# Kernel tuning notes

Measured on AMD Instinct MI355X. Metric: run time of the kernel, lower is better.

Reference implementation:

```python
import jax, jax.numpy as jnp
import numpy as np

B, H, W, C = 16, 32, 32, 256
N = H * W


def setup_inputs() -> dict:
    key = jax.random.key(0)
    ks = jax.random.split(key, 8)
    x = jax.random.normal(ks[0], (B, H, W, C), dtype=jnp.float32)
    # nn.LazyLinear(C): weight (C, C), bias (C,)
    scale = 1.0 / np.sqrt(C)
    Wq = jax.random.uniform(ks[1], (C, C), jnp.float32, -scale, scale)
    bq = jax.random.uniform(ks[2], (C,), jnp.float32, -scale, scale)
    Wk = jax.random.uniform(ks[3], (C, C), jnp.float32, -scale, scale)
    bk = jax.random.uniform(ks[4], (C,), jnp.float32, -scale, scale)
    Wv = jax.random.uniform(ks[5], (C, C), jnp.float32, -scale, scale)
    bv = jax.random.uniform(ks[6], (C,), jnp.float32, -scale, scale)
    # torch.randn(H, H*W, W)
    Wp = jax.random.normal(ks[7], (H, N, W), dtype=jnp.float32)
    return {"x": x, "Wq": Wq, "bq": bq, "Wk": Wk, "bk": bk,
            "Wv": Wv, "bv": bv, "Wp": Wp}


def reference(x, Wq, bq, Wk, bk, Wv, bv, Wp):
    b, h, w, c = x.shape
    n = h * w
    # Linear projections (torch Linear: x @ W^T + b), flatten spatial dims to N tokens
    q = (jnp.einsum('bhwc,dc->bhwd', x, Wq) + bq).reshape(b, n, c)
    k = (jnp.einsum('bhwc,dc->bhwd', x, Wk) + bk).reshape(b, n, c)
    v = (jnp.einsum('bhwc,dc->bhwd', x, Wv) + bv).reshape(b, n, c)
    # Unscaled attention over the N spatial tokens (no 1/sqrt(C) in the original)
    scores = jnp.einsum('bnc,bmc->bnm', q, k)          # (B, N, N)
    attn = jax.nn.softmax(scores, axis=-1)
    qkv = jnp.einsum('bnm,bmc->bnc', attn, v)           # (B, N, C)
    # z = (qkv^T [B,1,C,N] @ Wp [H,N,W]).transpose(-2,-1) -> (B, H, W, C)
    z = jnp.einsum('bnc,hnw->bhwc', qkv, Wp)
    return z
```

## Files before the change

### kernel.cpp

```cpp
#include <hip/hip_runtime.h>
#include <hip/hip_bf16.h>

#define BB 16
#define NN 1024
#define CC 256

typedef __attribute__((ext_vector_type(8))) short bf16x8;
typedef __attribute__((ext_vector_type(4))) float f32x4;

#define GPTR(p) ((const __attribute__((address_space(1))) void*)(p))
#define LPTR(p) ((__attribute__((address_space(3))) void*)(p))

__device__ __forceinline__ unsigned short f2bf(float f) {
  union { float f; unsigned u; } v; v.f = f;
  unsigned r = v.u + 0x7FFFu + ((v.u >> 16) & 1u);
  return (unsigned short)(r >> 16);
}

#define NCAST 17155
__global__ __launch_bounds__(256) void preprocess(
    const float* __restrict__ x,
    const float* __restrict__ Wq, const float* __restrict__ Wk,
    const float* __restrict__ Wv,
    const float* __restrict__ bq, const float* __restrict__ bk,
    const float* __restrict__ bv,
    const float* __restrict__ Wp,
    unsigned short* __restrict__ xb,
    unsigned short* __restrict__ wqkvb,
    float* __restrict__ bqkv,
    unsigned short* __restrict__ Amat) {
  __shared__ float tile[32][33];
  int blk = blockIdx.x;
  if (blk < NCAST) {
    const int NX = BB * NN * CC;
    const int NW = CC * CC;
    int i = blk * 256 + threadIdx.x;
    if (i < NX) { xb[i] = f2bf(x[i]); return; }
    int j = i - NX;
    if (j < 3 * NW) {
      const float* w = (j < NW) ? Wq : (j < 2 * NW ? Wk : Wv);
      wqkvb[j] = f2bf(w[j % NW]);
      return;
    }
    int jj = j - 3 * NW;
    if (jj < 3 * CC) {
      const float* bb = (jj < CC) ? bq : (jj < 2 * CC ? bk : bv);
      bqkv[jj] = bb[jj % CC];
    }
    return;
  }
  int wb = blk - NCAST;
  int h = wb >> 5;
  int n0 = (wb & 31) * 32;
#pragma unroll
  for (int j = 0; j < 4; j++) {
    int idx = threadIdx.x + j * 256;
    int a = idx >> 5, wc = idx & 31;
    tile[a][wc] = Wp[(size_t)h * (NN * 32) + (size_t)(n0 + a) * 32 + wc];
  }
  __syncthreads();
#pragma unroll
  for (int j = 0; j < 4; j++) {
    int idx = threadIdx.x + j * 256;
    int wc = idx >> 5, a = idx & 31;
    Amat[(size_t)(h * 32 + wc) * NN + n0 + a] = f2bf(tile[a][wc]);
  }
}

template <int BIAS_MODE, int F32OUT>
__global__ __launch_bounds__(256) void gemm_tile(
    const unsigned short* __restrict__ A, int lda, long sA,
    const unsigned short* __restrict__ Bt, int ldb, long sB,
    const float* __restrict__ bias,
    void* __restrict__ Out, int ldo, long sO, int K) {
  __shared__ unsigned short As[2 * 128 * 32];
  __shared__ unsigned short Bs[2 * 64 * 32];
  int b = blockIdx.x;
  int m0 = blockIdx.y * 128;
  int n0 = blockIdx.z * 64;
  int t = threadIdx.x;
  int w = t >> 6, lane = t & 63;
  int wm = (w >> 1) * 64, wn = (w & 1) * 32;
  int r = lane & 15, g = lane >> 4;

  const unsigned short* Ab = A + (long)b * sA;
  const unsigned short* Bb = Bt + (long)b * sB;

  int srow = t >> 2;
  int scol = (t & 3) * 8;

  f32x4 acc[4][2];
#pragma unroll
  for (int i = 0; i < 4; i++)
#pragma unroll
    for (int j = 0; j < 2; j++) acc[i][j] = (f32x4){0.f, 0.f, 0.f, 0.f};

  for (int k0 = 0; k0 < K; k0 += 64) {
    __syncthreads();
#pragma unroll
    for (int kh = 0; kh < 2; kh++) {
#pragma unroll
      for (int jj = 0; jj < 2; jj++) {
        __builtin_amdgcn_global_load_lds(
            GPTR(Ab + (long)(m0 + srow + jj * 64) * lda + k0 + kh * 32 + scol),
            LPTR(&As[kh * 4096 + jj * 2048 + t * 8]), 16, 0, 0);
      }
      __builtin_amdgcn_global_load_lds(
          GPTR(Bb + (long)(n0 + srow) * ldb + k0 + kh * 32 + scol),
          LPTR(&Bs[kh * 2048 + t * 8]), 16, 0, 0);
    }
    __syncthreads();
#pragma unroll
    for (int kh = 0; kh < 2; kh++) {
      bf16x8 af[4], bfr[2];
#pragma unroll
      for (int ti = 0; ti < 4; ti++)
        af[ti] = *(const bf16x8*)&As[kh * 4096 + (wm + ti * 16 + r) * 32 + g * 8];
#pragma unroll
      for (int tj = 0; tj < 2; tj++)
        bfr[tj] = *(const bf16x8*)&Bs[kh * 2048 + (wn + tj * 16 + r) * 32 + g * 8];
#pragma unroll
      for (int ti = 0; ti < 4; ti++)
#pragma unroll
        for (int tj = 0; tj < 2; tj++)
          acc[ti][tj] = __builtin_amdgcn_mfma_f32_16x16x32_bf16(af[ti], bfr[tj], acc[ti][tj], 0, 0, 0);
    }
  }

#pragma unroll
  for (int ti = 0; ti < 4; ti++) {
#pragma unroll
    for (int tj = 0; tj < 2; tj++) {
      int col = n0 + wn + tj * 16 + r;
      float bc = (BIAS_MODE == 1) ? bias[col] : 0.0f;
#pragma unroll
      for (int rr = 0; rr < 4; rr++) {
        int row = m0 + wm + ti * 16 + g * 4 + rr;
        float val = acc[ti][tj][rr] + bc;
        long oidx = (long)b * sO + (long)row * ldo + col;
        if (F32OUT)
          ((float*)Out)[oidx] = val;
        else
          ((unsigned short*)Out)[oidx] = f2bf(val);
      }
    }
  }
}

__global__ __launch_bounds__(256) void gemm_qkv(
    const unsigned short* __restrict__ A,
    const unsigned short* __restrict__ Bt,
    const float* __restrict__ bias,
    unsigned short* __restrict__ Qb, unsigned short* __restrict__ Kb,
    unsigned short* __restrict__ Vtb) {
  __shared__ unsigned short As[2 * 128 * 32];
  __shared__ unsigned short Bs[2 * 128 * 32];
  int b = blockIdx.x;
  int m0 = blockIdx.y * 128;
  int n0 = blockIdx.z * 128;
  int t = threadIdx.x;
  int w = t >> 6, lane = t & 63;
  int wm = (w >> 1) * 64, wn = (w & 1) * 64;
  int r = lane & 15, g = lane >> 4;

  const unsigned short* Ab = A + (long)b * NN * CC;
  int srow = t >> 2;
  int scol = (t & 3) * 8;

  f32x4 acc[4][4];
#pragma unroll
  for (int i = 0; i < 4; i++)
#pragma unroll
    for (int j = 0; j < 4; j++) acc[i][j] = (f32x4){0.f, 0.f, 0.f, 0.f};

  for (int k0 = 0; k0 < CC; k0 += 64) {
    __syncthreads();
#pragma unroll
    for (int kh = 0; kh < 2; kh++) {
#pragma unroll
      for (int jj = 0; jj < 2; jj++) {
        __builtin_amdgcn_global_load_lds(
            GPTR(Ab + (long)(m0 + srow + jj * 64) * CC + k0 + kh * 32 + scol),
            LPTR(&As[kh * 4096 + jj * 2048 + t * 8]), 16, 0, 0);
        __builtin_amdgcn_global_load_lds(
            GPTR(Bt + (long)(n0 + srow + jj * 64) * CC + k0 + kh * 32 + scol),
            LPTR(&Bs[kh * 4096 + jj * 2048 + t * 8]), 16, 0, 0);
      }
    }
    __syncthreads();
#pragma unroll
    for (int kh = 0; kh < 2; kh++) {
      bf16x8 af[4], bfr[4];
#pragma unroll
      for (int ti = 0; ti < 4; ti++)
        af[ti] = *(const bf16x8*)&As[kh * 4096 + (wm + ti * 16 + r) * 32 + g * 8];
#pragma unroll
      for (int tj = 0; tj < 4; tj++)
        bfr[tj] = *(const bf16x8*)&Bs[kh * 4096 + (wn + tj * 16 + r) * 32 + g * 8];
#pragma unroll
      for (int ti = 0; ti < 4; ti++)
#pragma unroll
        for (int tj = 0; tj < 4; tj++)
          acc[ti][tj] = __builtin_amdgcn_mfma_f32_16x16x32_bf16(af[ti], bfr[tj], acc[ti][tj], 0, 0, 0);
    }
  }

  int seg = n0 >> 8;
#pragma unroll
  for (int ti = 0; ti < 4; ti++) {
#pragma unroll
    for (int tj = 0; tj < 4; tj++) {
      int col = n0 + wn + tj * 16 + r;
      int c = col & 255;
      float bc = bias[col];
#pragma unroll
      for (int rr = 0; rr < 4; rr++) {
        int row = m0 + wm + ti * 16 + g * 4 + rr;
        float val = acc[ti][tj][rr] + bc;
        long base = (long)b * NN * CC;
        if (seg == 0) {
          Qb[base + (long)row * CC + c] = f2bf(val);
        } else if (seg == 1) {
          Kb[base + ((long)(c >> 5) * NN + row) * 32 + (c & 31)] = f2bf(val);
        } else {
          Vtb[base + ((((long)(c >> 4) * 128 + (row >> 3)) * 16 + (c & 15)) * 8 + (row & 7))] = f2bf(val);
        }
      }
    }
  }
}

__global__ __launch_bounds__(512, 4) void attn_fused(
    const unsigned short* __restrict__ Q,
    const unsigned short* __restrict__ Kt,
    const unsigned short* __restrict__ Vt,
    unsigned short* __restrict__ QKVt) {
  __shared__ unsigned short ShBuf[32 * 1024];
  __shared__ float red[8][32];
  int b = blockIdx.x;
  int n0 = blockIdx.y * 32;
  int t = threadIdx.x;
  int w = t >> 6, lane = t & 63;
  int r = lane & 15, g = lane >> 4;

  const unsigned short* kbase =
      Kt + (long)b * NN * CC + ((long)(w * 128 + r)) * 32 + g * 8;
  const unsigned short* qbase =
      Q + ((long)b * NN + n0 + r) * CC + g * 8;

  f32x4 acc[2][8];
#pragma unroll
  for (int i = 0; i < 2; i++)
#pragma unroll
    for (int j = 0; j < 8; j++) acc[i][j] = (f32x4){0.f, 0.f, 0.f, 0.f};

#pragma unroll
  for (int kk = 0; kk < 8; kk++) {
    bf16x8 qa0 = *(const bf16x8*)(qbase + kk * 32);
    bf16x8 qa1 = *(const bf16x8*)(qbase + 16 * CC + kk * 32);
    bf16x8 kf[8];
#pragma unroll
    for (int ct = 0; ct < 8; ct++)
      kf[ct] = *(const bf16x8*)(kbase + (long)kk * (NN * 32) + ct * 512);
#pragma unroll
    for (int ct = 0; ct < 8; ct++) {
      acc[0][ct] = __builtin_amdgcn_mfma_f32_16x16x32_bf16(qa0, kf[ct], acc[0][ct], 0, 0, 0);
      acc[1][ct] = __builtin_amdgcn_mfma_f32_16x16x32_bf16(qa1, kf[ct], acc[1][ct], 0, 0, 0);
    }
  }

  float mrow[2][4];
#pragma unroll
  for (int rt = 0; rt < 2; rt++) {
#pragma unroll
    for (int rr = 0; rr < 4; rr++) {
      float m = acc[rt][0][rr];
#pragma unroll
      for (int ct = 1; ct < 8; ct++) m = fmaxf(m, acc[rt][ct][rr]);
#pragma unroll
      for (int d = 1; d < 16; d <<= 1) m = fmaxf(m, __shfl_xor(m, d, 64));
      mrow[rt][rr] = m;
    }
  }
  if (r == 0) {
#pragma unroll
    for (int rt = 0; rt < 2; rt++)
#pragma unroll
      for (int rr = 0; rr < 4; rr++)
        red[w][rt * 16 + g * 4 + rr] = mrow[rt][rr];
  }
  __syncthreads();
#pragma unroll
  for (int rt = 0; rt < 2; rt++) {
#pragma unroll
    for (int rr = 0; rr < 4; rr++) {
      int row = rt * 16 + g * 4 + rr;
      float m = red[0][row];
#pragma unroll
      for (int w2 = 1; w2 < 8; w2++) m = fmaxf(m, red[w2][row]);
      mrow[rt][rr] = m;
    }
  }
  __syncthreads();
  float ssum[2][4];
#pragma unroll
  for (int rt = 0; rt < 2; rt++) {
#pragma unroll
    for (int rr = 0; rr < 4; rr++) {
      float s = 0.f;
#pragma unroll
      for (int ct = 0; ct < 8; ct++) {
        float e = exp2f((acc[rt][ct][rr] - mrow[rt][rr]) * 1.44269504088896f);
        acc[rt][ct][rr] = e;
        s += e;
      }
#pragma unroll
      for (int d = 1; d < 16; d <<= 1) s += __shfl_xor(s, d, 64);
      ssum[rt][rr] = s;
    }
  }
  if (r == 0) {
#pragma unroll
    for (int rt = 0; rt < 2; rt++)
#pragma unroll
      for (int rr = 0; rr < 4; rr++)
        red[w][rt * 16 + g * 4 + rr] = ssum[rt][rr];
  }
  __syncthreads();
#pragma unroll
  for (int rt = 0; rt < 2; rt++) {
#pragma unroll
    for (int rr = 0; rr < 4; rr++) {
      int row = rt * 16 + g * 4 + rr;
      float s = 0.f;
#pragma unroll
      for (int w2 = 0; w2 < 8; w2++) s += red[w2][row];
      float inv = 1.0f / s;
      int sw = row & 7;
#pragma unroll
      for (int ct = 0; ct < 8; ct++) {
        int col = w * 128 + ct * 16 + r;
        int chunk = (col >> 3) ^ sw;
        ShBuf[row * 1024 + chunk * 8 + (col & 7)] = f2bf(acc[rt][ct][rr] * inv);
      }
    }
  }
  __syncthreads();

  const unsigned short* vbase = Vt + (long)b * NN * CC;
  int cw = w * 32;
  f32x4 o[2][2];
#pragma unroll
  for (int i = 0; i < 2; i++)
#pragma unroll
    for (int j = 0; j < 2; j++) o[i][j] = (f32x4){0.f, 0.f, 0.f, 0.f};

#pragma unroll 4
  for (int m0 = 0; m0 < NN; m0 += 32) {
    bf16x8 ar[2], br[2];
#pragma unroll
    for (int bt = 0; bt < 2; bt++) {
      long vidx = (((long)((cw >> 4) + bt) * 128 + (m0 >> 3) + g) * 16 + r) * 8;
      br[bt] = *(const bf16x8*)(vbase + vidx);
    }
#pragma unroll
    for (int rt = 0; rt < 2; rt++) {
      int prow = rt * 16 + r;
      int chunk = ((m0 >> 3) + g) ^ (prow & 7);
      ar[rt] = *(const bf16x8*)&ShBuf[prow * 1024 + chunk * 8];
    }
#pragma unroll
    for (int rt = 0; rt < 2; rt++)
#pragma unroll
      for (int bt = 0; bt < 2; bt++)
        o[rt][bt] = __builtin_amdgcn_mfma_f32_16x16x32_bf16(ar[rt], br[bt], o[rt][bt], 0, 0, 0);
  }

  unsigned short* obase = QKVt + (long)b * NN * CC;
#pragma unroll
  for (int rt = 0; rt < 2; rt++) {
#pragma unroll
    for (int bt = 0; bt < 2; bt++) {
      int c = cw + bt * 16 + r;
#pragma unroll
      for (int rr = 0; rr < 4; rr++) {
        int n = n0 + rt * 16 + g * 4 + rr;
        obase[(long)c * NN + n] = f2bf(o[rt][bt][rr]);
      }
    }
  }
}

extern "C" void kernel_launch(void* const* d_in, const int* in_sizes, int n_in,
                              void* d_out, int out_size, void* d_ws, size_t ws_size,
                              hipStream_t stream) {
  const float* x  = (const float*)d_in[0];
  const float* Wq = (const float*)d_in[1];
  const float* bq = (const float*)d_in[2];
  const float* Wk = (const float*)d_in[3];
  const float* bk = (const float*)d_in[4];
  const float* Wv = (const float*)d_in[5];
  const float* bv = (const float*)d_in[6];
  const float* Wp = (const float*)d_in[7];
  float* out = (float*)d_out;

  const long BNC = (long)BB * NN * CC;

  char* p = (char*)d_ws;
  unsigned short* xb    = (unsigned short*)p; p += BNC * 2;
  unsigned short* wqkvb = (unsigned short*)p; p += 3L * CC * CC * 2;
  float*          bqkv  = (float*)p;          p += 4096;
  unsigned short* Amat  = (unsigned short*)p; p += (long)NN * NN * 2;
  unsigned short* Qb    = (unsigned short*)p; p += BNC * 2;
  unsigned short* Ktb   = (unsigned short*)p; p += BNC * 2;
  unsigned short* Vtb   = (unsigned short*)p; p += BNC * 2;
  unsigned short* QKVt  = (unsigned short*)p; p += BNC * 2;

  preprocess<<<NCAST + 1024, 256, 0, stream>>>(
      x, Wq, Wk, Wv, bq, bk, bv, Wp, xb, wqkvb, bqkv, Amat);

  gemm_qkv<<<dim3(BB, 8, 6), 256, 0, stream>>>(xb, wqkvb, bqkv, Qb, Ktb, Vtb);

  attn_fused<<<dim3(BB, NN / 32), 512, 0, stream>>>(Qb, Ktb, Vtb, QKVt);

  gemm_tile<0, 1><<<dim3(BB, 8, 4), 256, 0, stream>>>(
      Amat, NN, 0L, QKVt, NN, (long)NN * CC, nullptr,
      out, CC, (long)NN * CC, NN);
}
```

Before: 168.0 us.

## Double query rows per attention block and stream K through double-buffered LDS

Each attention block now handles 64 query rows instead of 32, which halves the number of blocks and halves K/V re-reads from global memory per query. K slices are copied into LDS with async global_load_lds into two buffers, so the load of the next slice overlaps the MFMAs on the current one, and Q fragments are prefetched one step ahead. Output stores are packed into 4-element vector writes. In exchange, LDS use and register pressure roughly double, occupancy drops (launch bounds 4 to 2, 128 KB of LDS), and the grid shrinks to 256 blocks.

New measurement: 156.0 us. 1.08x faster.

```diff
diff --git a/kernel.cpp b/kernel.cpp
--- a/kernel.cpp
+++ b/kernel.cpp
@@ -6,6 +6,7 @@
 #define CC 256
 
 typedef __attribute__((ext_vector_type(8))) short bf16x8;
+typedef __attribute__((ext_vector_type(4))) short s16x4;
 typedef __attribute__((ext_vector_type(4))) float f32x4;
 
 #define GPTR(p) ((const __attribute__((address_space(1))) void*)(p))
@@ -230,48 +231,78 @@
   }
 }
 
-__global__ __launch_bounds__(512, 4) void attn_fused(
+__global__ __launch_bounds__(512, 2) void attn_fused(
     const unsigned short* __restrict__ Q,
     const unsigned short* __restrict__ Kt,
     const unsigned short* __restrict__ Vt,
     unsigned short* __restrict__ QKVt) {
-  __shared__ unsigned short ShBuf[32 * 1024];
-  __shared__ float red[8][32];
+  __shared__ unsigned short ShBuf[64 * 1024];
+  __shared__ float red[8][64];
   int b = blockIdx.x;
-  int n0 = blockIdx.y * 32;
+  int n0 = blockIdx.y * 64;
   int t = threadIdx.x;
   int w = t >> 6, lane = t & 63;
   int r = lane & 15, g = lane >> 4;
 
-  const unsigned short* kbase =
-      Kt + (long)b * NN * CC + ((long)(w * 128 + r)) * 32 + g * 8;
-  const unsigned short* qbase =
-      Q + ((long)b * NN + n0 + r) * CC + g * 8;
-
-  f32x4 acc[2][8];
-#pragma unroll
-  for (int i = 0; i < 2; i++)
+  const unsigned short* kslab = Kt + (long)b * NN * CC + w * 128 * 32;
+  unsigned short* wbuf0 = &ShBuf[w * 4096];
+  unsigned short* wbuf1 = &ShBuf[32768 + w * 4096];
+
+  const unsigned short* qbase = Q + ((long)b * NN + n0 + r) * CC + g * 8;
+
+#pragma unroll
+  for (int j = 0; j < 8; j++)
+    __builtin_amdgcn_global_load_lds(GPTR(kslab + j * 512 + lane * 8),
+                                     LPTR(wbuf0 + j * 512 + lane * 8), 16, 0, 0);
+  bf16x8 qa[4];
+#pragma unroll
+  for (int rt = 0; rt < 4; rt++)
+    qa[rt] = *(const bf16x8*)(qbase + rt * 16 * CC);
+
+  f32x4 acc[4][8];
+#pragma unroll
+  for (int i = 0; i < 4; i++)
 #pragma unroll
     for (int j = 0; j < 8; j++) acc[i][j] = (f32x4){0.f, 0.f, 0.f, 0.f};
 
 #pragma unroll
   for (int kk = 0; kk < 8; kk++) {
-    bf16x8 qa0 = *(const bf16x8*)(qbase + kk * 32);
-    bf16x8 qa1 = *(const bf16x8*)(qbase + 16 * CC + kk * 32);
-    bf16x8 kf[8];
-#pragma unroll
-    for (int ct = 0; ct < 8; ct++)
-      kf[ct] = *(const bf16x8*)(kbase + (long)kk * (NN * 32) + ct * 512);
+    unsigned short* cur = (kk & 1) ? wbuf1 : wbuf0;
+    unsigned short* nxt = (kk & 1) ? wbuf0 : wbuf1;
+    if (kk < 7) {
+      const unsigned short* src = kslab + (long)(kk + 1) * (NN * 32);
+#pragma unroll
+      for (int j = 0; j < 8; j++)
+        __builtin_amdgcn_global_load_lds(GPTR(src + j * 512 + lane * 8),
+                                         LPTR(nxt + j * 512 + lane * 8), 16, 0, 0);
+      asm volatile("s_waitcnt vmcnt(8)" ::: "memory");
+    } else {
+      asm volatile("s_waitcnt vmcnt(0)" ::: "memory");
+    }
+    __builtin_amdgcn_sched_barrier(0);
+    bf16x8 qn[4];
+    if (kk < 7) {
+#pragma unroll
+      for (int rt = 0; rt < 4; rt++)
+        qn[rt] = *(const bf16x8*)(qbase + (kk + 1) * 32 + rt * 16 * CC);
+    }
 #pragma unroll
     for (int ct = 0; ct < 8; ct++) {
-      acc[0][ct] = __builtin_amdgcn_mfma_f32_16x16x32_bf16(qa0, kf[ct], acc[0][ct], 0, 0, 0);
-      acc[1][ct] = __builtin_amdgcn_mfma_f32_16x16x32_bf16(qa1, kf[ct], acc[1][ct], 0, 0, 0);
-    }
-  }
-
-  float mrow[2][4];
-#pragma unroll
-  for (int rt = 0; rt < 2; rt++) {
+      bf16x8 kf = *(const bf16x8*)&cur[(ct * 16 + r) * 32 + g * 8];
+#pragma unroll
+      for (int rt = 0; rt < 4; rt++)
+        acc[rt][ct] = __builtin_amdgcn_mfma_f32_16x16x32_bf16(qa[rt], kf, acc[rt][ct], 0, 0, 0);
+    }
+    if (kk < 7) {
+#pragma unroll
+      for (int rt = 0; rt < 4; rt++) qa[rt] = qn[rt];
+    }
+    __builtin_amdgcn_sched_barrier(0);
+  }
+
+  float mrow[4][4];
+#pragma unroll
+  for (int rt = 0; rt < 4; rt++) {
 #pragma unroll
     for (int rr = 0; rr < 4; rr++) {
       float m = acc[rt][0][rr];
@@ -284,14 +315,14 @@
   }
   if (r == 0) {
 #pragma unroll
-    for (int rt = 0; rt < 2; rt++)
+    for (int rt = 0; rt < 4; rt++)
 #pragma unroll
       for (int rr = 0; rr < 4; rr++)
         red[w][rt * 16 + g * 4 + rr] = mrow[rt][rr];
   }
   __syncthreads();
 #pragma unroll
-  for (int rt = 0; rt < 2; rt++) {
+  for (int rt = 0; rt < 4; rt++) {
 #pragma unroll
     for (int rr = 0; rr < 4; rr++) {
       int row = rt * 16 + g * 4 + rr;
@@ -302,9 +333,9 @@
     }
   }
   __syncthreads();
-  float ssum[2][4];
-#pragma unroll
-  for (int rt = 0; rt < 2; rt++) {
+  float ssum[4][4];
+#pragma unroll
+  for (int rt = 0; rt < 4; rt++) {
 #pragma unroll
     for (int rr = 0; rr < 4; rr++) {
       float s = 0.f;
@@ -321,27 +352,27 @@
   }
   if (r == 0) {
 #pragma unroll
-    for (int rt = 0; rt < 2; rt++)
+    for (int rt = 0; rt < 4; rt++)
 #pragma unroll
       for (int rr = 0; rr < 4; rr++)
         red[w][rt * 16 + g * 4 + rr] = ssum[rt][rr];
   }
   __syncthreads();
 #pragma unroll
-  for (int rt = 0; rt < 2; rt++) {
+  for (int rt = 0; rt < 4; rt++) {
 #pragma unroll
     for (int rr = 0; rr < 4; rr++) {
-      int row = rt * 16 + g * 4 + rr;
+      int prow = rt * 16 + g * 4 + rr;
       float s = 0.f;
 #pragma unroll
-      for (int w2 = 0; w2 < 8; w2++) s += red[w2][row];
+      for (int w2 = 0; w2 < 8; w2++) s += red[w2][prow];
       float inv = 1.0f / s;
-      int sw = row & 7;
+      int sw = prow & 7;
 #pragma unroll
       for (int ct = 0; ct < 8; ct++) {
         int col = w * 128 + ct * 16 + r;
         int chunk = (col >> 3) ^ sw;
-        ShBuf[row * 1024 + chunk * 8 + (col & 7)] = f2bf(acc[rt][ct][rr] * inv);
+        ShBuf[prow * 1024 + chunk * 8 + (col & 7)] = f2bf(acc[rt][ct][rr] * inv);
       }
     }
   }
@@ -349,28 +380,28 @@
 
   const unsigned short* vbase = Vt + (long)b * NN * CC;
   int cw = w * 32;
-  f32x4 o[2][2];
-#pragma unroll
-  for (int i = 0; i < 2; i++)
+  f32x4 o[4][2];
+#pragma unroll
+  for (int i = 0; i < 4; i++)
 #pragma unroll
     for (int j = 0; j < 2; j++) o[i][j] = (f32x4){0.f, 0.f, 0.f, 0.f};
 
 #pragma unroll 4
   for (int m0 = 0; m0 < NN; m0 += 32) {
-    bf16x8 ar[2], br[2];
+    bf16x8 ar[4], br[2];
 #pragma unroll
     for (int bt = 0; bt < 2; bt++) {
       long vidx = (((long)((cw >> 4) + bt) * 128 + (m0 >> 3) + g) * 16 + r) * 8;
       br[bt] = *(const bf16x8*)(vbase + vidx);
     }
 #pragma unroll
-    for (int rt = 0; rt < 2; rt++) {
+    for (int rt = 0; rt < 4; rt++) {
       int prow = rt * 16 + r;
       int chunk = ((m0 >> 3) + g) ^ (prow & 7);
       ar[rt] = *(const bf16x8*)&ShBuf[prow * 1024 + chunk * 8];
     }
 #pragma unroll
-    for (int rt = 0; rt < 2; rt++)
+    for (int rt = 0; rt < 4; rt++)
 #pragma unroll
       for (int bt = 0; bt < 2; bt++)
         o[rt][bt] = __builtin_amdgcn_mfma_f32_16x16x32_bf16(ar[rt], br[bt], o[rt][bt], 0, 0, 0);
@@ -378,15 +409,17 @@
 
   unsigned short* obase = QKVt + (long)b * NN * CC;
 #pragma unroll
-  for (int rt = 0; rt < 2; rt++) {
+  for (int rt = 0; rt < 4; rt++) {
 #pragma unroll
     for (int bt = 0; bt < 2; bt++) {
       int c = cw + bt * 16 + r;
-#pragma unroll
-      for (int rr = 0; rr < 4; rr++) {
-        int n = n0 + rt * 16 + g * 4 + rr;
-        obase[(long)c * NN + n] = f2bf(o[rt][bt][rr]);
-      }
+      int n = n0 + rt * 16 + g * 4;
+      s16x4 pk;
+      pk.x = (short)f2bf(o[rt][bt][0]);
+      pk.y = (short)f2bf(o[rt][bt][1]);
+      pk.z = (short)f2bf(o[rt][bt][2]);
+      pk.w = (short)f2bf(o[rt][bt][3]);
+      *(s16x4*)(obase + (long)c * NN + n) = pk;
     }
   }
 }
@@ -421,7 +454,7 @@
 
   gemm_qkv<<<dim3(BB, 8, 6), 256, 0, stream>>>(xb, wqkvb, bqkv, Qb, Ktb, Vtb);
 
-  attn_fused<<<dim3(BB, NN / 32), 512, 0, stream>>>(Qb, Ktb, Vtb, QKVt);
+  attn_fused<<<dim3(BB, NN / 64), 512, 0, stream>>>(Qb, Ktb, Vtb, QKVt);
 
   gemm_tile<0, 1><<<dim3(BB, 8, 4), 256, 0, stream>>>(
       Amat, NN, 0L, QKVt, NN, (long)NN * CC, nullptr,
```
